# Performance work log

Hardware: AMD Instinct MI355X
Metric: run time of the kernel (lower is better)

The kernel has to match this reference:

```python
import jax, jax.numpy as jnp
import numpy as np
from jax import lax

STRIDE = (1, 1)
PAD = ((1, 1), (1, 1))


def ste_sign(x, alpha):
    # Forward value is sign(x); backward flows through tanh(alpha*x) (STE).
    q = jnp.sign(x)
    e = jnp.tanh(alpha * x)
    return lax.stop_gradient(q - e) + e


def dwconv(x, w, channels):
    # x: [N,C,H,W], w: [C,1,k,j] (OIHW), depthwise => feature_group_count=C
    return lax.conv_general_dilated(
        x, w, window_strides=STRIDE, padding=PAD,
        dimension_numbers=("NCHW", "OIHW", "NCHW"),
        feature_group_count=channels)


def setup_inputs() -> dict:
    key = jax.random.key(0)
    k1, k2 = jax.random.split(key)
    x = jax.random.normal(k1, (32, 128, 112, 112), dtype=jnp.float32)
    weight = jax.random.normal(k2, (128, 1, 3, 3), dtype=jnp.float32)
    alpha_x = jnp.ones((), dtype=jnp.float32)
    alpha_w = jnp.ones((), dtype=jnp.float32)
    return {"x": x, "weight": weight, "alpha_x": alpha_x, "alpha_w": alpha_w}


def reference(x, weight, alpha_x, alpha_w):
    channels = weight.shape[0]
    xq = ste_sign(x, alpha_x)          # quantized activations (sign, STE)
    wq = ste_sign(weight, alpha_w)     # quantized weights (sign, STE)
    # out = dwconv(sign(x), w) + dwconv(x, sign(w)); matches the two einsums
    out = dwconv(xq, weight, channels) + dwconv(x, wq, channels)
    return out
```

## Files before the change

kernel.cpp:

```cpp
#include <hip/hip_runtime.h>


#define CH    128
#define HH    112
#define WW    112
#define NW4   28
#define PLANE (HH * WW)
#define RPT   7
#define NRG   (HH / RPT)
#define NTHR  (NW4 * NRG)

__device__ __forceinline__ float sgn(float v) {
    float one = __uint_as_float(0x3f800000u | (__float_as_uint(v) & 0x80000000u));
    return (v == 0.0f) ? 0.0f : one;
}

#define LOADROW(r, V)                                                 \
  {                                                                   \
    const int rr_ = (r);                                              \
    if (rr_ >= 0 && rr_ < HH) {                                       \
      const float* row_ = xc + rr_ * WW + col;                        \
      const float4 m_ = *reinterpret_cast<const float4*>(row_);       \
      V[1] = m_.x; V[2] = m_.y; V[3] = m_.z; V[4] = m_.w;             \
      V[0] = has_l ? row_[-1] : 0.0f;                                 \
      V[5] = has_r ? row_[4]  : 0.0f;                                 \
    } else {                                                          \
      V[0] = V[1] = V[2] = V[3] = V[4] = V[5] = 0.0f;                 \
    }                                                                 \
  }

#define SIGNROW(V, S)                                                 \
  { S[0]=sgn(V[0]); S[1]=sgn(V[1]); S[2]=sgn(V[2]);                   \
    S[3]=sgn(V[3]); S[4]=sgn(V[4]); S[5]=sgn(V[5]); }

#define ACCR(V, S, dr)                                                        \
    a0 = fmaf(S[0], W[3*(dr)+0], fmaf(V[0], Q[3*(dr)+0], a0));                \
    a0 = fmaf(S[1], W[3*(dr)+1], fmaf(V[1], Q[3*(dr)+1], a0));                \
    a0 = fmaf(S[2], W[3*(dr)+2], fmaf(V[2], Q[3*(dr)+2], a0));                \
    a1 = fmaf(S[1], W[3*(dr)+0], fmaf(V[1], Q[3*(dr)+0], a1));                \
    a1 = fmaf(S[2], W[3*(dr)+1], fmaf(V[2], Q[3*(dr)+1], a1));                \
    a1 = fmaf(S[3], W[3*(dr)+2], fmaf(V[3], Q[3*(dr)+2], a1));                \
    a2 = fmaf(S[2], W[3*(dr)+0], fmaf(V[2], Q[3*(dr)+0], a2));                \
    a2 = fmaf(S[3], W[3*(dr)+1], fmaf(V[3], Q[3*(dr)+1], a2));                \
    a2 = fmaf(S[4], W[3*(dr)+2], fmaf(V[4], Q[3*(dr)+2], a2));                \
    a3 = fmaf(S[3], W[3*(dr)+0], fmaf(V[3], Q[3*(dr)+0], a3));                \
    a3 = fmaf(S[4], W[3*(dr)+1], fmaf(V[4], Q[3*(dr)+1], a3));                \
    a3 = fmaf(S[5], W[3*(dr)+2], fmaf(V[5], Q[3*(dr)+2], a3));

#define STEP(i, VT, ST, VM, SM, VB, SB)                               \
  {                                                                   \
    LOADROW(rbase + (i) + 1, VB);                                     \
    SIGNROW(VB, SB);                                                  \
    float a0 = 0.f, a1 = 0.f, a2 = 0.f, a3 = 0.f;                     \
    ACCR(VT, ST, 0);                                                  \
    ACCR(VM, SM, 1);                                                  \
    ACCR(VB, SB, 2);                                                  \
    float4 o_; o_.x = a0; o_.y = a1; o_.z = a2; o_.w = a3;            \
    *reinterpret_cast<float4*>(oc + (rbase + (i)) * WW + col) = o_;   \
  }

__global__ __launch_bounds__(NTHR) void bisign_dwconv_kernel(
    const float* __restrict__ x,
    const float* __restrict__ wt,
    float* __restrict__ out)
{
    const int plane = blockIdx.x;
    const int c = plane & (CH - 1);

    const float* __restrict__ xc = x   + (size_t)plane * PLANE;
    float* __restrict__       oc = out + (size_t)plane * PLANE;

    float W[9], Q[9];
#pragma unroll
    for (int k = 0; k < 9; ++k) {
        const float wv = wt[c * 9 + k];
        W[k] = wv;
        Q[k] = sgn(wv);
    }

    const int tid   = threadIdx.x;
    const int col4  = tid % NW4;
    const int rg    = tid / NW4;
    const int col   = col4 * 4;
    const int rbase = rg * RPT;

    const bool has_l = (col4 > 0);
    const bool has_r = (col4 < NW4 - 1);

    float V0[6], V1[6], V2[6], S0[6], S1[6], S2[6];

    LOADROW(rbase - 1, V0); SIGNROW(V0, S0);
    LOADROW(rbase,     V1); SIGNROW(V1, S1);

    STEP(0, V0, S0, V1, S1, V2, S2);
    STEP(1, V1, S1, V2, S2, V0, S0);
    STEP(2, V2, S2, V0, S0, V1, S1);
    STEP(3, V0, S0, V1, S1, V2, S2);
    STEP(4, V1, S1, V2, S2, V0, S0);
    STEP(5, V2, S2, V0, S0, V1, S1);
    STEP(6, V0, S0, V1, S1, V2, S2);
}

extern "C" void kernel_launch(void* const* d_in, const int* in_sizes, int n_in,
                              void* d_out, int out_size, void* d_ws, size_t ws_size,
                              hipStream_t stream) {
    const float* x  = (const float*)d_in[0];
    const float* wt = (const float*)d_in[1];
    float* out = (float*)d_out;

    const int N = in_sizes[0] / (CH * PLANE);
    const int nblocks = N * CH;

    bisign_dwconv_kernel<<<nblocks, NTHR, 0, stream>>>(x, wt, out);
}
```

Before: 358.4 us.

## Use wavefront shuffles for halo columns and prefetch rows two ahead

Threads are remapped so each row uses 32 lanes (28 active columns plus padding). The left and right halo values now come from neighbouring lanes through __shfl_up and __shfl_down instead of separate scalar global loads. Row loads are issued one step ahead, so each load overlaps with the current FMA work, and interior rows skip the bounds checks. In exchange, 4 of every 32 lanes do redundant work, the block grows from 448 to 512 threads, and more registers are needed to hold the prefetched rows.

```diff
diff --git a/kernel.cpp b/kernel.cpp
--- a/kernel.cpp
+++ b/kernel.cpp
@@ -5,33 +5,39 @@
 #define HH    112
 #define WW    112
 #define NW4   28
+#define LPR   32
 #define PLANE (HH * WW)
 #define RPT   7
-#define NRG   (HH / RPT)
-#define NTHR  (NW4 * NRG)
+#define NRG   16
+#define NTHR  (LPR * NRG)
 
 __device__ __forceinline__ float sgn(float v) {
     float one = __uint_as_float(0x3f800000u | (__float_as_uint(v) & 0x80000000u));
     return (v == 0.0f) ? 0.0f : one;
 }
 
-#define LOADROW(r, V)                                                 \
+#define LOAD_SAFE(r, M)                                               \
+    M = *reinterpret_cast<const float4*>(xc + (r) * WW + col);
+
+#define LOAD_EDGE(r, M)                                               \
   {                                                                   \
-    const int rr_ = (r);                                              \
-    if (rr_ >= 0 && rr_ < HH) {                                       \
-      const float* row_ = xc + rr_ * WW + col;                        \
-      const float4 m_ = *reinterpret_cast<const float4*>(row_);       \
-      V[1] = m_.x; V[2] = m_.y; V[3] = m_.z; V[4] = m_.w;             \
-      V[0] = has_l ? row_[-1] : 0.0f;                                 \
-      V[5] = has_r ? row_[4]  : 0.0f;                                 \
-    } else {                                                          \
-      V[0] = V[1] = V[2] = V[3] = V[4] = V[5] = 0.0f;                 \
-    }                                                                 \
+    const int rr_  = ((r) < 0) ? 0 : (((r) > HH - 1) ? HH - 1 : (r)); \
+    const bool ob_ = ((r) < 0) | ((r) > HH - 1);                      \
+    M = *reinterpret_cast<const float4*>(xc + rr_ * WW + col);        \
+    M.x = ob_ ? 0.f : M.x;  M.y = ob_ ? 0.f : M.y;                    \
+    M.z = ob_ ? 0.f : M.z;  M.w = ob_ ? 0.f : M.w;                    \
   }
 
-#define SIGNROW(V, S)                                                 \
-  { S[0]=sgn(V[0]); S[1]=sgn(V[1]); S[2]=sgn(V[2]);                   \
-    S[3]=sgn(V[3]); S[4]=sgn(V[4]); S[5]=sgn(V[5]); }
+#define EXPAND(M, V, S)                                               \
+  {                                                                   \
+    V[1] = M.x; V[2] = M.y; V[3] = M.z; V[4] = M.w;                   \
+    const float up_ = __shfl_up(M.w, 1, 64);                          \
+    const float dn_ = __shfl_down(M.x, 1, 64);                        \
+    V[0] = (col4 == 0)       ? 0.f : up_;                             \
+    V[5] = (col4 == NW4 - 1) ? 0.f : dn_;                             \
+    S[0] = sgn(V[0]); S[1] = sgn(V[1]); S[2] = sgn(V[2]);             \
+    S[3] = sgn(V[3]); S[4] = sgn(V[4]); S[5] = sgn(V[5]);             \
+  }
 
 #define ACCR(V, S, dr)                                                        \
     a0 = fmaf(S[0], W[3*(dr)+0], fmaf(V[0], Q[3*(dr)+0], a0));                \
@@ -47,16 +53,18 @@
     a3 = fmaf(S[4], W[3*(dr)+1], fmaf(V[4], Q[3*(dr)+1], a3));                \
     a3 = fmaf(S[5], W[3*(dr)+2], fmaf(V[5], Q[3*(dr)+2], a3));
 
-#define STEP(i, VT, ST, VM, SM, VB, SB)                               \
+#define STEP(i, PRE, EXP, EVt, ESt, EVm, ESm, EVb, ESb)               \
   {                                                                   \
-    LOADROW(rbase + (i) + 1, VB);                                     \
-    SIGNROW(VB, SB);                                                  \
+    PRE;                                                              \
+    EXP;                                                              \
     float a0 = 0.f, a1 = 0.f, a2 = 0.f, a3 = 0.f;                     \
-    ACCR(VT, ST, 0);                                                  \
-    ACCR(VM, SM, 1);                                                  \
-    ACCR(VB, SB, 2);                                                  \
-    float4 o_; o_.x = a0; o_.y = a1; o_.z = a2; o_.w = a3;            \
-    *reinterpret_cast<float4*>(oc + (rbase + (i)) * WW + col) = o_;   \
+    ACCR(EVt, ESt, 0);                                                \
+    ACCR(EVm, ESm, 1);                                                \
+    ACCR(EVb, ESb, 2);                                                \
+    if (col4 < NW4) {                                                 \
+      float4 o_; o_.x = a0; o_.y = a1; o_.z = a2; o_.w = a3;          \
+      *reinterpret_cast<float4*>(oc + (rbase + (i)) * WW + col) = o_; \
+    }                                                                 \
   }
 
 __global__ __launch_bounds__(NTHR) void bisign_dwconv_kernel(
@@ -79,26 +87,28 @@
     }
 
     const int tid   = threadIdx.x;
-    const int col4  = tid % NW4;
-    const int rg    = tid / NW4;
-    const int col   = col4 * 4;
-    const int rbase = rg * RPT;
+    const int col4  = tid & (LPR - 1);
+    const int rseg  = tid >> 5;
+    const int col4c = (col4 < NW4 - 1) ? col4 : NW4 - 1;
+    const int col   = col4c * 4;
+    const int rbase = rseg * RPT;
 
-    const bool has_l = (col4 > 0);
-    const bool has_r = (col4 < NW4 - 1);
+    float4 MA, MB, MC, MD;
+    float EAv[6], EAs[6], EBv[6], EBs[6], ECv[6], ECs[6];
 
-    float V0[6], V1[6], V2[6], S0[6], S1[6], S2[6];
+    LOAD_EDGE(rbase - 1, MA);
+    LOAD_SAFE(rbase,     MB);
+    LOAD_SAFE(rbase + 1, MC);
+    EXPAND(MA, EAv, EAs);
+    EXPAND(MB, EBv, EBs);
 
-    LOADROW(rbase - 1, V0); SIGNROW(V0, S0);
-    LOADROW(rbase,     V1); SIGNROW(V1, S1);
-
-    STEP(0, V0, S0, V1, S1, V2, S2);
-    STEP(1, V1, S1, V2, S2, V0, S0);
-    STEP(2, V2, S2, V0, S0, V1, S1);
-    STEP(3, V0, S0, V1, S1, V2, S2);
-    STEP(4, V1, S1, V2, S2, V0, S0);
-    STEP(5, V2, S2, V0, S0, V1, S1);
-    STEP(6, V0, S0, V1, S1, V2, S2);
+    STEP(0, LOAD_SAFE(rbase + 2, MD), EXPAND(MC, ECv, ECs), EAv, EAs, EBv, EBs, ECv, ECs);
+    STEP(1, LOAD_SAFE(rbase + 3, MA), EXPAND(MD, EAv, EAs), EBv, EBs, ECv, ECs, EAv, EAs);
+    STEP(2, LOAD_SAFE(rbase + 4, MB), EXPAND(MA, EBv, EBs), ECv, ECs, EAv, EAs, EBv, EBs);
+    STEP(3, LOAD_SAFE(rbase + 5, MC), EXPAND(MB, ECv, ECs), EAv, EAs, EBv, EBs, ECv, ECs);
+    STEP(4, LOAD_SAFE(rbase + 6, MD), EXPAND(MC, EAv, EAs), EBv, EBs, ECv, ECs, EAv, EAs);
+    STEP(5, LOAD_EDGE(rbase + 7, MA), EXPAND(MD, EBv, EBs), ECv, ECs, EAv, EAs, EBv, EBs);
+    STEP(6, ((void)0),                EXPAND(MA, ECv, ECs), EAv, EAs, EBv, EBs, ECv, ECs);
 }
 
 extern "C" void kernel_launch(void* const* d_in, const int* in_sizes, int n_in,
```

Result: faster. 348.5 us (-2.8%).
